# Kernel tuning notes

Hardware: AMD Instinct MI355X
Metric: run time of the kernel (lower is better)

## Reference

```python
import jax, jax.numpy as jnp
import numpy as np

KS = 5          # B-spline kernel_size per pseudo-coordinate dim
DIM = 2         # pseudo-coordinate dimensionality
NUM_GRAPHS = 64


def spline_conv(x, src, dst, edge_attr, W, root, bias):
    """Degree-1 open B-spline conv (torch-spline-conv semantics, aggr='mean').
    x: [N,Cin], edge_attr: [E,DIM] in [0,1], W: [KS**DIM,Cin,Cout]."""
    N = x.shape[0]
    E = src.shape[0]
    v = edge_attr * (KS - 1)                                   # [E,DIM]
    k_lo = jnp.clip(jnp.floor(v), 0, KS - 2).astype(jnp.int32) # lower knot index
    frac = v - k_lo.astype(v.dtype)                            # [E,DIM]
    # Precompute x @ W_k for all K kernel weights per node: [N,K,Cout]
    xW = jnp.einsum('nc,kco->nko', x, W)
    msg = jnp.zeros((E, W.shape[2]), x.dtype)
    # 2^DIM = 4 nonzero basis products for degree-1 splines
    for bits in ((0, 0), (0, 1), (1, 0), (1, 1)):
        b = jnp.ones((E,), x.dtype)
        wi = jnp.zeros((E,), jnp.int32)
        stride = 1
        for d, bit in enumerate(bits):
            b = b * (frac[:, d] if bit else (1.0 - frac[:, d]))
            wi = wi + (k_lo[:, d] + bit) * stride
            stride *= KS
        msg = msg + b[:, None] * xW[src, wi]                   # gather [E,Cout]
    agg = jax.ops.segment_sum(msg, dst, num_segments=N)
    deg = jax.ops.segment_sum(jnp.ones((E,), x.dtype), dst, num_segments=N)
    agg = agg / jnp.maximum(deg, 1.0)[:, None]                 # mean aggregation
    return agg + x @ root + bias


def setup_inputs() -> dict:
    key = jax.random.key(0)
    ks = jax.random.split(key, 12)
    N, E = 20000, 320000
    Cin, H, O = 1, 32, 10
    K = KS * KS
    p = lambda k, s: jax.random.normal(k, s, jnp.float32) * 0.1
    return {
        'x': jax.random.normal(ks[0], (N, Cin), jnp.float32),
        'edge_attr': jax.random.uniform(ks[1], (E, DIM), jnp.float32),
        'W1': p(ks[2], (K, Cin, H)), 'root1': p(ks[3], (Cin, H)), 'b1': jnp.zeros((H,), jnp.float32),
        'W2': p(ks[4], (K, H, 2 * H)), 'root2': p(ks[5], (H, 2 * H)), 'b2': jnp.zeros((2 * H,), jnp.float32),
        'Wf1': p(ks[6], (2 * H, 128)), 'bf1': jnp.zeros((128,), jnp.float32),
        'Wf2': p(ks[7], (128, O)), 'bf2': jnp.zeros((O,), jnp.float32),
        'edge_index': jax.random.randint(ks[8], (2, E), 0, N),
        'batch': jnp.sort(jax.random.randint(ks[9], (N,), 0, NUM_GRAPHS)),
    }


def reference(x, edge_attr, W1, root1, b1, W2, root2, b2, Wf1, bf1, Wf2, bf2, edge_index, batch):
    src, dst = edge_index[0], edge_index[1]
    h = jax.nn.relu(spline_conv(x, src, dst, edge_attr, W1, root1, b1))
    h = jax.nn.relu(spline_conv(h, src, dst, edge_attr, W2, root2, b2))
    # global mean pool over graphs
    gsum = jax.ops.segment_sum(h, batch, num_segments=NUM_GRAPHS)
    cnt = jax.ops.segment_sum(jnp.ones((h.shape[0],), h.dtype), batch, num_segments=NUM_GRAPHS)
    g = gsum / jnp.maximum(cnt, 1.0)[:, None]
    g = jax.nn.relu(g @ Wf1 + bf1)
    return jax.nn.log_softmax(g @ Wf2 + bf2, axis=1)
```

## Files before the change

### kernel.cpp

```cpp
#include <hip/hip_runtime.h>
#include <hip/hip_fp16.h>
#include <math.h>

#define KK 25
#define H1C 32
#define H2C 64
#define FCC 128
#define NCLS 10
#define NG 64
#define M1 32
#define M2 16
#define NHB 128
#define HBIN 10240

typedef _Float16 v8h __attribute__((ext_vector_type(8)));
typedef float v4f __attribute__((ext_vector_type(4)));

__global__ __launch_bounds__(256) void hist_kernel(
    const int* __restrict__ edge_index, int E, int N,
    int* __restrict__ part) {
    __shared__ int hs[HBIN];
    int b = blockIdx.x, tid = threadIdx.x;
    int per = (E + NHB - 1) / NHB;
    int beg = b * per, end = min(E, beg + per);
    for (int lo = 0; lo < N; lo += HBIN) {
        int sz = min(HBIN, N - lo);
        __syncthreads();
        for (int i = tid; i < sz; i += 256) hs[i] = 0;
        __syncthreads();
        for (int i = beg + tid; i < end; i += 256) {
            int d = edge_index[E + i] - lo;
            if ((unsigned)d < (unsigned)sz) atomicAdd(&hs[d], 1);
        }
        __syncthreads();
        for (int i = tid; i < sz; i += 256) part[(size_t)b * N + lo + i] = hs[i];
    }
}

__global__ void merge_kernel(const int* __restrict__ part, int N,
                             int* __restrict__ degi) {
    int n = blockIdx.x * 256 + threadIdx.x;
    if (n >= N) return;
    int s = 0;
    for (int b = 0; b < NHB; b++) s += part[(size_t)b * N + n];
    degi[n] = s;
}

__global__ void scan1_kernel(const int* __restrict__ degi, int N,
                             int* __restrict__ incl, int* __restrict__ bsum) {
    __shared__ int s[256];
    int tid = threadIdx.x;
    int i = blockIdx.x * 256 + tid;
    int v = (i < N) ? degi[i] : 0;
    s[tid] = v;
    __syncthreads();
    for (int off = 1; off < 256; off <<= 1) {
        int t = (tid >= off) ? s[tid - off] : 0;
        __syncthreads();
        s[tid] += t;
        __syncthreads();
    }
    if (i < N) incl[i] = s[tid];
    if (tid == 255) bsum[blockIdx.x] = s[255];
}

__global__ void scan2_kernel(int* __restrict__ bsum, int nb) {
    __shared__ int s[256];
    int tid = threadIdx.x;
    int v = (tid < nb) ? bsum[tid] : 0;
    s[tid] = v;
    __syncthreads();
    for (int off = 1; off < 256; off <<= 1) {
        int t = (tid >= off) ? s[tid - off] : 0;
        __syncthreads();
        s[tid] += t;
        __syncthreads();
    }
    if (tid < nb) bsum[tid] = s[tid] - v;
}

__global__ void scan3_kernel(const int* __restrict__ incl, const int* __restrict__ degi,
                             const int* __restrict__ bsum, int N,
                             int* __restrict__ rowst, int* __restrict__ cur) {
    int i = blockIdx.x * 256 + threadIdx.x;
    if (i >= N) return;
    int r = incl[i] - degi[i] + bsum[blockIdx.x];
    rowst[i] = r;
    cur[i] = r;
}

__global__ void bucket_kernel(const float* __restrict__ edge_attr,
                              const int* __restrict__ edge_index, int E,
                              int* __restrict__ cur, int4* __restrict__ es) {
    int e = blockIdx.x * blockDim.x + threadIdx.x;
    if (e >= E) return;
    float v0 = edge_attr[2 * e + 0] * 4.0f;
    float v1 = edge_attr[2 * e + 1] * 4.0f;
    int k0 = (int)floorf(v0); k0 = min(max(k0, 0), 3);
    int k1 = (int)floorf(v1); k1 = min(max(k1, 0), 3);
    float f0 = v0 - (float)k0, f1 = v1 - (float)k1;
    int dst = edge_index[E + e];
    int pos = atomicAdd(&cur[dst], 1);
    es[pos] = make_int4(edge_index[e], (dst << 8) | (k0 + 5 * k1),
                        __float_as_int(f0), __float_as_int(f1));
}

__global__ void w2t_kernel(const float* __restrict__ W2, __half* __restrict__ W2t) {
    int idx = blockIdx.x * 256 + threadIdx.x;
    if (idx >= KK * H2C * H1C) return;
    int c = idx & 31, o = (idx >> 5) & 63, k = idx >> 11;
    W2t[idx] = __float2half(W2[(k * H1C + c) * H2C + o]);
}

__global__ __launch_bounds__(256) void l1_kernel(
    const float* __restrict__ x,
    const int* __restrict__ rowst, const int* __restrict__ degi,
    const int4* __restrict__ es,
    const float* __restrict__ W1, const float* __restrict__ root1,
    const float* __restrict__ b1, int N, int E,
    float* __restrict__ h1, __half* __restrict__ h1f) {
    __shared__ float w1s[KK * H1C];
    __shared__ float agg1[M1 * H1C];
    __shared__ int4 eb[8][32];
    __shared__ float xb[8][32];
    int tid = threadIdx.x;
    for (int i = tid; i < KK * H1C; i += 256) w1s[i] = W1[i];
    for (int i = tid; i < M1 * H1C; i += 256) agg1[i] = 0.0f;
    __syncthreads();
    int g = tid >> 5, o = tid & 31;
    int n0 = blockIdx.x * M1;
    int blkBeg = rowst[n0];
    int blkEnd = (n0 + M1 < N) ? rowst[n0 + M1] : E;
    int total = blkEnd - blkBeg;
    int per = (total + 7) >> 3;
    int wBeg = blkBeg + g * per;
    int wEnd = min(blkEnd, wBeg + per);
    int curDst = -1;
    float acc = 0.0f;
    for (int base = wBeg; base < wEnd; base += 32) {
        int m = min(32, wEnd - base);
        if (o < m) {
            int4 ed = es[base + o];
            eb[g][o] = ed;
            xb[g][o] = x[ed.x];
        }
        for (int j = 0; j < m; j++) {
            int4 ed = eb[g][j];
            float xs = xb[g][j];
            int dst = ed.y >> 8;
            if (dst != curDst) {
                if (curDst >= 0) atomicAdd(&agg1[(curDst - n0) * H1C + o], acc);
                acc = 0.0f;
                curDst = dst;
            }
            float f0 = __int_as_float(ed.z), f1 = __int_as_float(ed.w);
            float g0 = 1.0f - f0, g1 = 1.0f - f1;
            int kb = (ed.y & 0xff) << 5;
            float coef = g0 * g1 * w1s[kb + o] + f0 * g1 * w1s[kb + 32 + o] +
                         g0 * f1 * w1s[kb + 160 + o] + f0 * f1 * w1s[kb + 192 + o];
            acc = fmaf(xs, coef, acc);
        }
    }
    if (curDst >= 0) atomicAdd(&agg1[(curDst - n0) * H1C + o], acc);
    __syncthreads();
#pragma unroll
    for (int i = 0; i < 4; i++) {
        int ln = g + 8 * i;
        int n = n0 + ln;
        if (n < N) {
            float rdeg = 1.0f / fmaxf((float)degi[n], 1.0f);
            float hv = fmaxf(agg1[ln * H1C + o] * rdeg + x[n] * root1[o] + b1[o], 0.0f);
            h1[n * H1C + o] = hv;
            h1f[n * H1C + o] = __float2half(hv);
        }
    }
}

__global__ __launch_bounds__(256) void xw2m_kernel(
    const __half* __restrict__ h1f,
    const __half* __restrict__ W2t,
    int N, __half* __restrict__ xph) {
    int wv = threadIdx.x >> 6;
    int lane = threadIdx.x & 63;
    int r15 = lane & 15, quad = lane >> 4;
    int n0 = blockIdx.x * 16;
    int o0 = wv * 16;
    v8h afrag = {};
    int an = n0 + r15;
    if (an < N) afrag = *(const v8h*)(h1f + (size_t)an * H1C + quad * 8);
    for (int k = 0; k < KK; k++) {
        v8h bfrag = *(const v8h*)(W2t + ((k << 6) + o0 + r15) * H1C + quad * 8);
        v4f acc = {};
        acc = __builtin_amdgcn_mfma_f32_16x16x32_f16(afrag, bfrag, acc, 0, 0, 0);
#pragma unroll
        for (int r = 0; r < 4; r++) {
            int mn = n0 + quad * 4 + r;
            if (mn < N)
                xph[(size_t)mn * (KK * H2C) + (k << 6) + o0 + r15] = __float2half(acc[r]);
        }
    }
}

__global__ __launch_bounds__(256) void l2_kernel(
    const float* __restrict__ h1,
    const int* __restrict__ rowst, const int* __restrict__ degi,
    const int4* __restrict__ es,
    const unsigned* __restrict__ xphu,
    const float* __restrict__ root2, const float* __restrict__ b2,
    const int* __restrict__ batch,
    int N, int E, float* __restrict__ gsum) {
    __shared__ float agg[M2 * H2C];
    __shared__ int4 eb[4][64];
    int tid = threadIdx.x;
    for (int i = tid; i < M2 * H2C; i += 256) agg[i] = 0.0f;
    __syncthreads();
    int w = tid >> 6, lane = tid & 63;
    int o2 = lane & 31, eh = lane >> 5;
    int n0 = blockIdx.x * M2;
    int blkBeg = rowst[n0];
    int blkEnd = (n0 + M2 < N) ? rowst[n0 + M2] : E;
    int total = blkEnd - blkBeg;
    int per = (total + 3) >> 2;
    int wBeg = blkBeg + w * per;
    int wEnd = min(blkEnd, wBeg + per);
    int curDst = -1;
    float ax = 0.0f, ay = 0.0f;
    for (int base = wBeg; base < wEnd; base += 64) {
        int m = min(64, wEnd - base);
        if (lane < m) eb[w][lane] = es[base + lane];
        for (int j = 0; j < m; j += 2) {
            int jj = j + eh;
            bool act = jj < m;
            int4 ed = eb[w][act ? jj : j];
            const unsigned* p = xphu + (size_t)ed.x * (KK * H2C / 2) +
                                ((ed.y & 0xff) << 5) + o2;
            unsigned t0 = p[0], t1 = p[32], t2 = p[160], t3 = p[192];
            if (act) {
                int dst = ed.y >> 8;
                if (dst != curDst) {
                    if (curDst >= 0) {
                        atomicAdd(&agg[(curDst - n0) * H2C + 2 * o2], ax);
                        atomicAdd(&agg[(curDst - n0) * H2C + 2 * o2 + 1], ay);
                    }
                    ax = ay = 0.0f;
                    curDst = dst;
                }
                float f0 = __int_as_float(ed.z), f1 = __int_as_float(ed.w);
                float g0 = 1.0f - f0, g1 = 1.0f - f1;
                float b0 = g0 * g1, b1 = f0 * g1, bb2 = g0 * f1, b3 = f0 * f1;
                __half2 h0 = *(__half2*)&t0, h1v = *(__half2*)&t1;
                __half2 h2 = *(__half2*)&t2, h3 = *(__half2*)&t3;
                ax = fmaf(b0, __low2float(h0), ax);  ay = fmaf(b0, __high2float(h0), ay);
                ax = fmaf(b1, __low2float(h1v), ax); ay = fmaf(b1, __high2float(h1v), ay);
                ax = fmaf(bb2, __low2float(h2), ax); ay = fmaf(bb2, __high2float(h2), ay);
                ax = fmaf(b3, __low2float(h3), ax);  ay = fmaf(b3, __high2float(h3), ay);
            }
        }
    }
    if (curDst >= 0) {
        atomicAdd(&agg[(curDst - n0) * H2C + 2 * o2], ax);
        atomicAdd(&agg[(curDst - n0) * H2C + 2 * o2 + 1], ay);
    }
    __syncthreads();

#pragma unroll
    for (int i = 0; i < 4; i++) {
        int ln = w + 4 * i;
        int n = n0 + ln;
        if (n < N) {
            float rd = 1.0f / fmaxf((float)degi[n], 1.0f);
            float v = agg[ln * H2C + lane] * rd + b2[lane];
            const float* hr = h1 + n * H1C;
#pragma unroll 8
            for (int c = 0; c < H1C; c++) v = fmaf(hr[c], root2[c * H2C + lane], v);
            agg[ln * H2C + lane] = fmaxf(v, 0.0f);
        } else {
            agg[ln * H2C + lane] = 0.0f;
        }
    }
    __syncthreads();

    if (tid < H2C) {
        float run = 0.0f;
        int curg = batch[n0];
        for (int ln = 0; ln < M2; ln++) {
            int n = n0 + ln;
            if (n >= N) break;
            int gg = batch[n];
            if (gg != curg) {
                atomicAdd(&gsum[curg * H2C + tid], run);
                run = 0.0f;
                curg = gg;
            }
            run += agg[ln * H2C + tid];
        }
        atomicAdd(&gsum[curg * H2C + tid], run);
    }
}

__global__ void head_kernel(const float* __restrict__ gsum,
                            const int* __restrict__ batch, int N,
                            const float* __restrict__ Wf1, const float* __restrict__ bf1,
                            const float* __restrict__ Wf2, const float* __restrict__ bf2,
                            float* __restrict__ out) {
    __shared__ float gc[H2C];
    __shared__ float t1[FCC];
    __shared__ float lg[NCLS];
    __shared__ float lse;
    __shared__ float scnt;
    int g = blockIdx.x, tid = threadIdx.x;
    if (tid == 0) {
        int lo = 0, hi = N;
        while (lo < hi) { int m = (lo + hi) >> 1; if (batch[m] < g) lo = m + 1; else hi = m; }
        int lb = lo;
        lo = 0; hi = N;
        while (lo < hi) { int m = (lo + hi) >> 1; if (batch[m] <= g) lo = m + 1; else hi = m; }
        scnt = (float)(lo - lb);
    }
    __syncthreads();
    if (tid < H2C) gc[tid] = gsum[g * H2C + tid] / fmaxf(scnt, 1.0f);
    __syncthreads();
    {
        float acc = bf1[tid];
        for (int c = 0; c < H2C; c++) acc += gc[c] * Wf1[c * FCC + tid];
        t1[tid] = fmaxf(acc, 0.0f);
    }
    __syncthreads();
    if (tid < NCLS) {
        float acc = bf2[tid];
        for (int j = 0; j < FCC; j++) acc += t1[j] * Wf2[j * NCLS + tid];
        lg[tid] = acc;
    }
    __syncthreads();
    if (tid == 0) {
        float m = lg[0];
        for (int c = 1; c < NCLS; c++) m = fmaxf(m, lg[c]);
        float s = 0.0f;
        for (int c = 0; c < NCLS; c++) s += expf(lg[c] - m);
        lse = m + logf(s);
    }
    __syncthreads();
    if (tid < NCLS) out[g * NCLS + tid] = lg[tid] - lse;
}

extern "C" void kernel_launch(void* const* d_in, const int* in_sizes, int n_in,
                              void* d_out, int out_size, void* d_ws, size_t ws_size,
                              hipStream_t stream) {
    const float* x          = (const float*)d_in[0];
    const float* edge_attr  = (const float*)d_in[1];
    const float* W1         = (const float*)d_in[2];
    const float* root1      = (const float*)d_in[3];
    const float* b1         = (const float*)d_in[4];
    const float* W2         = (const float*)d_in[5];
    const float* root2      = (const float*)d_in[6];
    const float* b2         = (const float*)d_in[7];
    const float* Wf1        = (const float*)d_in[8];
    const float* bf1        = (const float*)d_in[9];
    const float* Wf2        = (const float*)d_in[10];
    const float* bf2        = (const float*)d_in[11];
    const int*   edge_index = (const int*)d_in[12];
    const int*   batch      = (const int*)d_in[13];
    float* out = (float*)d_out;

    const int N = in_sizes[13];
    const int E = in_sizes[12] / 2;
    const int NB = (N + 255) / 256;

    int4*     es   = (int4*)d_ws;
    unsigned* xphu = (unsigned*)(es + E);
    __half*   w2t  = (__half*)(xphu + (size_t)N * 800);
    __half*   h1f  = w2t + KK * H2C * H1C;
    float* gsum  = (float*)(h1f + (size_t)N * H1C);
    int*   degi  = (int*)(gsum + NG * H2C);
    int*   rowst = degi + N;
    int*   cur   = rowst + N;
    int*   incl  = cur + N;
    int*   bsum  = incl + N;
    float* h1    = (float*)(bsum + 256);
    int*   part  = (int*)(h1 + (size_t)N * H1C);

    hipMemsetAsync(gsum, 0, (size_t)NG * H2C * sizeof(float), stream);

    hist_kernel<<<NHB, 256, 0, stream>>>(edge_index, E, N, part);
    merge_kernel<<<NB, 256, 0, stream>>>(part, N, degi);

    scan1_kernel<<<NB, 256, 0, stream>>>(degi, N, incl, bsum);
    scan2_kernel<<<1, 256, 0, stream>>>(bsum, NB);
    scan3_kernel<<<NB, 256, 0, stream>>>(incl, degi, bsum, N, rowst, cur);

    bucket_kernel<<<(E + 255) / 256, 256, 0, stream>>>(edge_attr, edge_index, E, cur, es);
    w2t_kernel<<<(KK * H2C * H1C + 255) / 256, 256, 0, stream>>>(W2, w2t);

    l1_kernel<<<(N + M1 - 1) / M1, 256, 0, stream>>>(
        x, rowst, degi, es, W1, root1, b1, N, E, h1, h1f);

    xw2m_kernel<<<(N + 15) / 16, 256, 0, stream>>>(h1f, w2t, N, (__half*)xphu);

    l2_kernel<<<(N + M2 - 1) / M2, 256, 0, stream>>>(
        h1, rowst, degi, es, xphu, root2, b2, batch, N, E, gsum);

    head_kernel<<<NG, FCC, 0, stream>>>(gsum, batch, N, Wf1, bf1, Wf2, bf2, out);
}
```

Baseline: 214.0 us.

## Bucket edges via per-block shared histograms and flatten edge loops with LDS atomics

Replaces the global-atomic bucketing pass with a two-stage counting sort: per-block offsets come from the existing partial histograms, and each block scatters its edges using shared-memory atomics. This removes contended global atomics on the cursor array. The layer-1 and layer-2 aggregation loops drop the per-warp dst run tracking and instead stage edge chunks block-wide and atomically add each edge's contribution into shared accumulators. Layer 2 also splits the four basis terms across half-waves, so each lane does two loads instead of four. In exchange there are more LDS atomics and extra block syncs per chunk.

```diff
diff --git a/kernel.cpp b/kernel.cpp
--- a/kernel.cpp
+++ b/kernel.cpp
@@ -12,6 +12,8 @@
 #define M2 16
 #define NHB 128
 #define HBIN 10240
+#define ECH1 256
+#define ECH2 256
 
 typedef _Float16 v8h __attribute__((ext_vector_type(8)));
 typedef float v4f __attribute__((ext_vector_type(4)));
@@ -42,6 +44,7 @@
     int n = blockIdx.x * 256 + threadIdx.x;
     if (n >= N) return;
     int s = 0;
+#pragma unroll 8
     for (int b = 0; b < NHB; b++) s += part[(size_t)b * N + n];
     degi[n] = s;
 }
@@ -81,28 +84,52 @@
 
 __global__ void scan3_kernel(const int* __restrict__ incl, const int* __restrict__ degi,
                              const int* __restrict__ bsum, int N,
-                             int* __restrict__ rowst, int* __restrict__ cur) {
+                             int* __restrict__ rowst) {
     int i = blockIdx.x * 256 + threadIdx.x;
     if (i >= N) return;
-    int r = incl[i] - degi[i] + bsum[blockIdx.x];
-    rowst[i] = r;
-    cur[i] = r;
-}
-
-__global__ void bucket_kernel(const float* __restrict__ edge_attr,
-                              const int* __restrict__ edge_index, int E,
-                              int* __restrict__ cur, int4* __restrict__ es) {
-    int e = blockIdx.x * blockDim.x + threadIdx.x;
-    if (e >= E) return;
-    float v0 = edge_attr[2 * e + 0] * 4.0f;
-    float v1 = edge_attr[2 * e + 1] * 4.0f;
-    int k0 = (int)floorf(v0); k0 = min(max(k0, 0), 3);
-    int k1 = (int)floorf(v1); k1 = min(max(k1, 0), 3);
-    float f0 = v0 - (float)k0, f1 = v1 - (float)k1;
-    int dst = edge_index[E + e];
-    int pos = atomicAdd(&cur[dst], 1);
-    es[pos] = make_int4(edge_index[e], (dst << 8) | (k0 + 5 * k1),
-                        __float_as_int(f0), __float_as_int(f1));
+    rowst[i] = incl[i] - degi[i] + bsum[blockIdx.x];
+}
+
+__global__ void offs_kernel(const int* __restrict__ rowst, int N,
+                            int* __restrict__ part) {
+    int n = blockIdx.x * 256 + threadIdx.x;
+    if (n >= N) return;
+    int run = rowst[n];
+#pragma unroll 8
+    for (int b = 0; b < NHB; b++) {
+        int t = part[(size_t)b * N + n];
+        part[(size_t)b * N + n] = run;
+        run += t;
+    }
+}
+
+__global__ __launch_bounds__(256) void bucket2_kernel(
+    const float* __restrict__ edge_attr, const int* __restrict__ edge_index,
+    int E, int N, int* __restrict__ part, int4* __restrict__ es) {
+    __shared__ int hs[HBIN];
+    int b = blockIdx.x, tid = threadIdx.x;
+    int per = (E + NHB - 1) / NHB;
+    int beg = b * per, end = min(E, beg + per);
+    for (int lo = 0; lo < N; lo += HBIN) {
+        int sz = min(HBIN, N - lo);
+        __syncthreads();
+        for (int i = tid; i < sz; i += 256) hs[i] = part[(size_t)b * N + lo + i];
+        __syncthreads();
+        for (int e = beg + tid; e < end; e += 256) {
+            int dst = edge_index[E + e];
+            int d = dst - lo;
+            if ((unsigned)d < (unsigned)sz) {
+                int pos = atomicAdd(&hs[d], 1);
+                float v0 = edge_attr[2 * e + 0] * 4.0f;
+                float v1 = edge_attr[2 * e + 1] * 4.0f;
+                int k0 = min(max((int)floorf(v0), 0), 3);
+                int k1 = min(max((int)floorf(v1), 0), 3);
+                float f0 = v0 - (float)k0, f1 = v1 - (float)k1;
+                es[pos] = make_int4(edge_index[e], (dst << 8) | (k0 + 5 * k1),
+                                    __float_as_int(f0), __float_as_int(f1));
+            }
+        }
+    }
 }
 
 __global__ void w2t_kernel(const float* __restrict__ W2, __half* __restrict__ W2t) {
@@ -121,51 +148,40 @@
     float* __restrict__ h1, __half* __restrict__ h1f) {
     __shared__ float w1s[KK * H1C];
     __shared__ float agg1[M1 * H1C];
-    __shared__ int4 eb[8][32];
-    __shared__ float xb[8][32];
+    __shared__ int4 eb[ECH1];
+    __shared__ float xb[ECH1];
     int tid = threadIdx.x;
     for (int i = tid; i < KK * H1C; i += 256) w1s[i] = W1[i];
     for (int i = tid; i < M1 * H1C; i += 256) agg1[i] = 0.0f;
-    __syncthreads();
-    int g = tid >> 5, o = tid & 31;
+    int h = tid >> 5, o = tid & 31;
     int n0 = blockIdx.x * M1;
     int blkBeg = rowst[n0];
     int blkEnd = (n0 + M1 < N) ? rowst[n0 + M1] : E;
-    int total = blkEnd - blkBeg;
-    int per = (total + 7) >> 3;
-    int wBeg = blkBeg + g * per;
-    int wEnd = min(blkEnd, wBeg + per);
-    int curDst = -1;
-    float acc = 0.0f;
-    for (int base = wBeg; base < wEnd; base += 32) {
-        int m = min(32, wEnd - base);
-        if (o < m) {
-            int4 ed = es[base + o];
-            eb[g][o] = ed;
-            xb[g][o] = x[ed.x];
-        }
-        for (int j = 0; j < m; j++) {
-            int4 ed = eb[g][j];
-            float xs = xb[g][j];
-            int dst = ed.y >> 8;
-            if (dst != curDst) {
-                if (curDst >= 0) atomicAdd(&agg1[(curDst - n0) * H1C + o], acc);
-                acc = 0.0f;
-                curDst = dst;
-            }
+    for (int base = blkBeg; base < blkEnd; base += ECH1) {
+        int m = min(ECH1, blkEnd - base);
+        __syncthreads();
+        for (int i = tid; i < m; i += 256) {
+            int4 ed = es[base + i];
+            eb[i] = ed;
+            xb[i] = x[ed.x];
+        }
+        __syncthreads();
+#pragma unroll 2
+        for (int i = h; i < m; i += 8) {
+            int4 ed = eb[i];
+            float xs = xb[i];
             float f0 = __int_as_float(ed.z), f1 = __int_as_float(ed.w);
             float g0 = 1.0f - f0, g1 = 1.0f - f1;
             int kb = (ed.y & 0xff) << 5;
             float coef = g0 * g1 * w1s[kb + o] + f0 * g1 * w1s[kb + 32 + o] +
                          g0 * f1 * w1s[kb + 160 + o] + f0 * f1 * w1s[kb + 192 + o];
-            acc = fmaf(xs, coef, acc);
-        }
-    }
-    if (curDst >= 0) atomicAdd(&agg1[(curDst - n0) * H1C + o], acc);
+            atomicAdd(&agg1[((ed.y >> 8) - n0) * H1C + o], xs * coef);
+        }
+    }
     __syncthreads();
 #pragma unroll
     for (int i = 0; i < 4; i++) {
-        int ln = g + 8 * i;
+        int ln = h + 8 * i;
         int n = n0 + ln;
         if (n < N) {
             float rdeg = 1.0f / fmaxf((float)degi[n], 1.0f);
@@ -210,56 +226,35 @@
     const int* __restrict__ batch,
     int N, int E, float* __restrict__ gsum) {
     __shared__ float agg[M2 * H2C];
-    __shared__ int4 eb[4][64];
+    __shared__ int4 eb[ECH2];
     int tid = threadIdx.x;
     for (int i = tid; i < M2 * H2C; i += 256) agg[i] = 0.0f;
-    __syncthreads();
     int w = tid >> 6, lane = tid & 63;
-    int o2 = lane & 31, eh = lane >> 5;
+    int j = lane >> 5, o2 = lane & 31;
     int n0 = blockIdx.x * M2;
     int blkBeg = rowst[n0];
     int blkEnd = (n0 + M2 < N) ? rowst[n0 + M2] : E;
-    int total = blkEnd - blkBeg;
-    int per = (total + 3) >> 2;
-    int wBeg = blkBeg + w * per;
-    int wEnd = min(blkEnd, wBeg + per);
-    int curDst = -1;
-    float ax = 0.0f, ay = 0.0f;
-    for (int base = wBeg; base < wEnd; base += 64) {
-        int m = min(64, wEnd - base);
-        if (lane < m) eb[w][lane] = es[base + lane];
-        for (int j = 0; j < m; j += 2) {
-            int jj = j + eh;
-            bool act = jj < m;
-            int4 ed = eb[w][act ? jj : j];
-            const unsigned* p = xphu + (size_t)ed.x * (KK * H2C / 2) +
-                                ((ed.y & 0xff) << 5) + o2;
-            unsigned t0 = p[0], t1 = p[32], t2 = p[160], t3 = p[192];
-            if (act) {
-                int dst = ed.y >> 8;
-                if (dst != curDst) {
-                    if (curDst >= 0) {
-                        atomicAdd(&agg[(curDst - n0) * H2C + 2 * o2], ax);
-                        atomicAdd(&agg[(curDst - n0) * H2C + 2 * o2 + 1], ay);
-                    }
-                    ax = ay = 0.0f;
-                    curDst = dst;
-                }
-                float f0 = __int_as_float(ed.z), f1 = __int_as_float(ed.w);
-                float g0 = 1.0f - f0, g1 = 1.0f - f1;
-                float b0 = g0 * g1, b1 = f0 * g1, bb2 = g0 * f1, b3 = f0 * f1;
-                __half2 h0 = *(__half2*)&t0, h1v = *(__half2*)&t1;
-                __half2 h2 = *(__half2*)&t2, h3 = *(__half2*)&t3;
-                ax = fmaf(b0, __low2float(h0), ax);  ay = fmaf(b0, __high2float(h0), ay);
-                ax = fmaf(b1, __low2float(h1v), ax); ay = fmaf(b1, __high2float(h1v), ay);
-                ax = fmaf(bb2, __low2float(h2), ax); ay = fmaf(bb2, __high2float(h2), ay);
-                ax = fmaf(b3, __low2float(h3), ax);  ay = fmaf(b3, __high2float(h3), ay);
-            }
-        }
-    }
-    if (curDst >= 0) {
-        atomicAdd(&agg[(curDst - n0) * H2C + 2 * o2], ax);
-        atomicAdd(&agg[(curDst - n0) * H2C + 2 * o2 + 1], ay);
+    for (int base = blkBeg; base < blkEnd; base += ECH2) {
+        int m = min(ECH2, blkEnd - base);
+        __syncthreads();
+        for (int i = tid; i < m; i += 256) eb[i] = es[base + i];
+        __syncthreads();
+#pragma unroll 2
+        for (int i = w; i < m; i += 4) {
+            int4 ed = eb[i];
+            const unsigned* p = xphu + (size_t)ed.x * 800 + ((ed.y & 0xff) << 5) + lane;
+            unsigned tA = p[0];
+            unsigned tB = p[160];
+            float f0 = __int_as_float(ed.z), f1 = __int_as_float(ed.w);
+            float blo = j ? f0 : (1.0f - f0);
+            float g1v = 1.0f - f1;
+            __half2 hA = *(__half2*)&tA, hB = *(__half2*)&tB;
+            float vx = blo * fmaf(g1v, __low2float(hA), f1 * __low2float(hB));
+            float vy = blo * fmaf(g1v, __high2float(hA), f1 * __high2float(hB));
+            int dl = (ed.y >> 8) - n0;
+            atomicAdd(&agg[dl * H2C + 2 * o2], vx);
+            atomicAdd(&agg[dl * H2C + 2 * o2 + 1], vy);
+        }
     }
     __syncthreads();
 
@@ -373,8 +368,7 @@
     float* gsum  = (float*)(h1f + (size_t)N * H1C);
     int*   degi  = (int*)(gsum + NG * H2C);
     int*   rowst = degi + N;
-    int*   cur   = rowst + N;
-    int*   incl  = cur + N;
+    int*   incl  = rowst + N;
     int*   bsum  = incl + N;
     float* h1    = (float*)(bsum + 256);
     int*   part  = (int*)(h1 + (size_t)N * H1C);
@@ -386,9 +380,11 @@
 
     scan1_kernel<<<NB, 256, 0, stream>>>(degi, N, incl, bsum);
     scan2_kernel<<<1, 256, 0, stream>>>(bsum, NB);
-    scan3_kernel<<<NB, 256, 0, stream>>>(incl, degi, bsum, N, rowst, cur);
-
-    bucket_kernel<<<(E + 255) / 256, 256, 0, stream>>>(edge_attr, edge_index, E, cur, es);
+    scan3_kernel<<<NB, 256, 0, stream>>>(incl, degi, bsum, N, rowst);
+
+    offs_kernel<<<NB, 256, 0, stream>>>(rowst, N, part);
+    bucket2_kernel<<<NHB, 256, 0, stream>>>(edge_attr, edge_index, E, N, part, es);
+
     w2t_kernel<<<(KK * H2C * H1C + 255) / 256, 256, 0, stream>>>(W2, w2t);
 
     l1_kernel<<<(N + M1 - 1) / M1, 256, 0, stream>>>(
```

New measurement: 478.5 us. 2.24x slower.
